# Kernel optimization log

Measured on AMD Instinct MI355X. Metric: run time of the kernel, lower is better.

Reference implementation:

```python
import jax, jax.numpy as jnp
import numpy as np

HIDDEN = 1024
H2 = HIDDEN // 2
LAYERS = 2
NUM_CONDS = 4


def _lstm_dir(x, Wih, Whh, b, reverse):
    # x: (B, T, I); Wih: (4*H2, I); Whh: (4*H2, H2); b: (4*H2,)
    B = x.shape[0]
    h2 = Whh.shape[1]
    pre = jnp.einsum('bti,gi->btg', x, Wih) + b  # precompute input contribution
    pre = jnp.swapaxes(pre, 0, 1)  # (T, B, 4*H2)
    if reverse:
        pre = pre[::-1]

    def step(carry, g_in):
        h, c = carry
        g = g_in + h @ Whh.T
        i, f, gg, o = jnp.split(g, 4, axis=-1)
        c = jax.nn.sigmoid(f) * c + jax.nn.sigmoid(i) * jnp.tanh(gg)
        h = jax.nn.sigmoid(o) * jnp.tanh(c)
        return (h, c), h

    init = (jnp.zeros((B, h2), x.dtype), jnp.zeros((B, h2), x.dtype))
    _, hs = jax.lax.scan(step, init, pre)
    if reverse:
        hs = hs[::-1]
    return jnp.swapaxes(hs, 0, 1)  # (B, T, H2)


def _bilstm(x, Wih, Whh, b):
    # Wih: (L, 2, 4*H2, I) — all layers share input width since embed_dim == hidden_dim
    out = x
    for l in range(Wih.shape[0]):
        fwd = _lstm_dir(out, Wih[l, 0], Whh[l, 0], b[l, 0], False)
        bwd = _lstm_dir(out, Wih[l, 1], Whh[l, 1], b[l, 1], True)
        out = jnp.concatenate([fwd, bwd], axis=-1)
    return out


def setup_inputs() -> dict:
    key = jax.random.key(0)
    ks = jax.random.split(key, 24)
    s = 0.02
    G = 4 * H2
    inp = {
        'question_embedding': jax.random.normal(ks[0], (32, 128, 1024), jnp.float32),
        'packed_column_embedding': jax.random.normal(ks[1], (640, 8, 1024), jnp.float32),
        'gold_num': jax.random.randint(ks[2], (32,), 0, 5),
        'gold_cols': jax.random.randint(ks[3], (32, 4), 0, 20),
        'gold_ops': jax.random.randint(ks[4], (32, 4), 0, 4),
        'num_columns': 20,
        'q_Wih': jax.random.normal(ks[5], (LAYERS, 2, G, 1024), jnp.float32) * s,
        'q_Whh': jax.random.normal(ks[6], (LAYERS, 2, G, H2), jnp.float32) * s,
        'q_b': jax.random.normal(ks[7], (LAYERS, 2, G), jnp.float32) * s,
        'c_Wih': jax.random.normal(ks[8], (LAYERS, 2, G, 1024), jnp.float32) * s,
        'c_Whh': jax.random.normal(ks[9], (LAYERS, 2, G, H2), jnp.float32) * s,
        'c_b': jax.random.normal(ks[10], (LAYERS, 2, G), jnp.float32) * s,
        'col_attn_w': jax.random.normal(ks[11], (1, HIDDEN), jnp.float32) * s,
        'col_attn_b': jnp.zeros((1,), jnp.float32),
        'ob_attn_W': jax.random.normal(ks[12], (HIDDEN, HIDDEN), jnp.float32) * s,
        'ob_attn_b': jnp.zeros((HIDDEN,), jnp.float32),
        'ob_col_W': jax.random.normal(ks[13], (HIDDEN, HIDDEN), jnp.float32) * s,
        'ob_col_b': jnp.zeros((HIDDEN,), jnp.float32),
        'q_proj_W': jax.random.normal(ks[14], (HIDDEN, HIDDEN), jnp.float32) * s,
        'q_proj_b': jnp.zeros((HIDDEN,), jnp.float32),
        'out1_W': jax.random.normal(ks[15], (HIDDEN, 3 * HIDDEN), jnp.float32) * s,
        'out1_b': jnp.zeros((HIDDEN,), jnp.float32),
        'out2_W': jax.random.normal(ks[16], (2, HIDDEN), jnp.float32) * s,
        'out2_b': jnp.zeros((2,), jnp.float32),
    }
    return inp


def _forward(question_embedding, packed_column_embedding, gold_num, gold_cols,
             num_columns, q_Wih, q_Whh, q_b, c_Wih, c_Whh, c_b,
             col_attn_w, col_attn_b, ob_attn_W, ob_attn_b, ob_col_W, ob_col_b,
             q_proj_W, q_proj_b, out1_W, out1_b, out2_W, out2_b):
    dt = question_embedding.dtype
    bs, Tq, _ = question_embedding.shape
    # compute_mask: nonzero token positions
    q_mask = (jnp.abs(question_embedding).sum(-1) != 0).astype(dt)  # (B, Tq)
    c_mask = (jnp.abs(packed_column_embedding).sum(-1) != 0).astype(dt)  # (P, Tc)

    q_enc = _bilstm(question_embedding, q_Wih, q_Whh, q_b)  # (B, Tq, H)
    c_enc = _bilstm(packed_column_embedding, c_Wih, c_Whh, c_b)  # (P, Tc, H)

    # attention-pool each column name: make_weight = masked softmax over tokens
    logits = jnp.einsum('pth,oh->pt', c_enc, col_attn_w) + col_attn_b[0]
    logits = jnp.where(c_mask > 0, logits, -jnp.inf)
    w = jax.nn.softmax(logits, axis=-1)
    col_pooled = jnp.einsum('pt,pth->ph', w, c_enc)  # (P, H)
    column_hidden = col_pooled.reshape(bs, num_columns, HIDDEN)  # (B, NC, H)

    # get_observed_column_hidden (torch.no_grad): gather gold columns, zero-pad
    K = gold_cols.shape[1]
    gn = jnp.minimum(gold_num, K)
    cond_mask = (jnp.arange(K)[None, :] < gn[:, None]).astype(dt)  # (B, K)
    observed = jnp.take_along_axis(column_hidden, gold_cols[:, :, None], axis=1)  # (B, K, H)
    observed = observed * cond_mask[..., None]
    observed = jax.lax.stop_gradient(observed)
    cond_mask = jax.lax.stop_gradient(cond_mask)

    # mm_attention over question tokens
    att_key = observed @ ob_attn_W.T + ob_attn_b  # (B, K, H)
    scores = jnp.einsum('bkh,bqh->bkq', att_key, q_enc)
    scores = jnp.where(q_mask[:, None, :] > 0, scores, -jnp.inf)
    attn = jax.nn.softmax(scores, axis=-1)
    q_hidden = jnp.einsum('bkq,bqh->bkh', attn, q_enc)  # (B, K, H)

    vec = jnp.concatenate([observed @ ob_col_W.T + ob_col_b,
                           q_hidden @ q_proj_W.T + q_proj_b], axis=-1)  # (B, K, 2H)
    # broadcast concat: (B, K, Tq, 3H)
    x = jnp.concatenate([
        jnp.broadcast_to(q_enc[:, None], (bs, K, Tq, HIDDEN)),
        jnp.broadcast_to(vec[:, :, None], (bs, K, Tq, 2 * HIDDEN)),
    ], axis=-1)
    h1 = jnp.tanh(x @ out1_W.T + out1_b)
    pos = h1 @ out2_W.T + out2_b  # (B, K, Tq, 2)

    full_mask = cond_mask[:, :, None] * q_mask[:, None, :]  # (B, K, Tq)
    pos = jnp.where(full_mask[..., None] > 0, pos, -jnp.inf)
    return pos[..., 0], pos[..., 1]


def reference(question_embedding, packed_column_embedding, gold_num, gold_cols,
              gold_ops, num_columns, q_Wih, q_Whh, q_b, c_Wih, c_Whh, c_b,
              col_attn_w, col_attn_b, ob_attn_W, ob_attn_b, ob_col_W, ob_col_b,
              q_proj_W, q_proj_b, out1_W, out1_b, out2_W, out2_b):
    # gold_ops is accepted but unused by the original forward
    return _forward(question_embedding, packed_column_embedding, gold_num, gold_cols,
                    num_columns, q_Wih, q_Whh, q_b, c_Wih, c_Whh, c_b,
                    col_attn_w, col_attn_b, ob_attn_W, ob_attn_b, ob_col_W, ob_col_b,
                    q_proj_W, q_proj_b, out1_W, out1_b, out2_W, out2_b)
```

## Files before the change

### kernel.cpp

```cpp
#include <hip/hip_runtime.h>
#include <math.h>


using f32x4 = __attribute__((ext_vector_type(4))) float;
using s16x8 = __attribute__((ext_vector_type(8))) short;
typedef unsigned long long ulong_t;

#define ASYNC_COPY16(gsrc, ldst)                                               \
  __builtin_amdgcn_global_load_lds(                                            \
      (const __attribute__((address_space(1))) void*)(gsrc),                   \
      (__attribute__((address_space(3))) void*)(ldst), 16, 0, 0)

static __device__ __forceinline__ float sigm(float x) {
  return 1.0f / (1.0f + expf(-x));
}

static __device__ __forceinline__ unsigned short f2b_one(float x) {
  unsigned int u = __float_as_uint(x);
  u = (u + 0x7FFFu + ((u >> 16) & 1u)) >> 16;
  return (unsigned short)u;
}

static __device__ __forceinline__ bool haszero16(ulong_t x) {
  return ((x - 0x0001000100010001ull) & ~x & 0x8000800080008000ull) != 0ull;
}

#define SENT64 0x7FC07FC07FC07FC0ull

__global__ __launch_bounds__(256) void f2b_kernel(
    const float* __restrict__ in, unsigned short* __restrict__ out, int n4)
{
  const int i = blockIdx.x * 256 + threadIdx.x;
  if (i >= n4) return;
  const float4 v = ((const float4*)in)[i];
  ushort4 r;
  r.x = f2b_one(v.x); r.y = f2b_one(v.y);
  r.z = f2b_one(v.z); r.w = f2b_one(v.w);
  ((ushort4*)out)[i] = r;
}

__global__ __launch_bounds__(256) void mask_kernel(
    const float* __restrict__ qe, const float* __restrict__ pce,
    float* __restrict__ qmask, float* __restrict__ cmask)
{
  const int w = threadIdx.x >> 6;
  const int lane = threadIdx.x & 63;
  const int row = blockIdx.x * 4 + w;
  const float* src = (row < 4096) ? (qe + (size_t)row * 1024)
                                  : (pce + (size_t)(row - 4096) * 1024);
  float s = 0.f;
#pragma unroll
  for (int j = 0; j < 16; ++j) s += fabsf(src[lane + j * 64]);
#pragma unroll
  for (int off = 32; off > 0; off >>= 1) s += __shfl_down(s, off, 64);
  if (lane == 0) {
    const float m = (s != 0.f) ? 1.f : 0.f;
    if (row < 4096) qmask[row] = m;
    else cmask[row - 4096] = m;
  }
}

__global__ __launch_bounds__(256) void mfma_gemm_kernel(
    const unsigned short* __restrict__ X, const unsigned short* __restrict__ W,
    const float* __restrict__ bias, float* __restrict__ C,
    int K, int ldx, int ldw, int k0w, int ldc, int c0)
{
  __shared__ unsigned short As[128 * 32];
  __shared__ unsigned short Bs[128 * 32];
  const int tid = threadIdx.x;
  const int w = tid >> 6;
  const int l = tid & 63;
  const int m0 = blockIdx.y * 128;
  const int n0 = blockIdx.x * 128;
  const int wm = (w >> 1) * 64;
  const int wn = (w & 1) * 64;

  const unsigned short* xg =
      X + (size_t)(m0 + w * 32 + (l >> 2)) * ldx + (l & 3) * 8;
  const unsigned short* wgp =
      W + (size_t)(n0 + w * 32 + (l >> 2)) * ldw + k0w + (l & 3) * 8;
  unsigned short* asb = As + w * 1024;
  unsigned short* bsb = Bs + w * 1024;

  const int fr = l & 15;
  const int fq = l >> 4;
  const unsigned short* aRd = As + (wm + fr) * 32 + fq * 8;
  const unsigned short* bRd = Bs + (wn + fr) * 32 + fq * 8;

  f32x4 acc[4][4];
#pragma unroll
  for (int i = 0; i < 4; ++i)
#pragma unroll
    for (int j = 0; j < 4; ++j) acc[i][j] = (f32x4){0.f, 0.f, 0.f, 0.f};

  for (int k0 = 0; k0 < K; k0 += 32) {
    ASYNC_COPY16(xg + k0, asb);
    ASYNC_COPY16(xg + (size_t)16 * ldx + k0, asb + 512);
    ASYNC_COPY16(wgp + k0, bsb);
    ASYNC_COPY16(wgp + (size_t)16 * ldw + k0, bsb + 512);
    __syncthreads();
    s16x8 a[4], b[4];
#pragma unroll
    for (int i = 0; i < 4; ++i) a[i] = *(const s16x8*)(aRd + i * 512);
#pragma unroll
    for (int j = 0; j < 4; ++j) b[j] = *(const s16x8*)(bRd + j * 512);
#pragma unroll
    for (int i = 0; i < 4; ++i)
#pragma unroll
      for (int j = 0; j < 4; ++j)
        acc[i][j] = __builtin_amdgcn_mfma_f32_16x16x32_bf16(
            a[i], b[j], acc[i][j], 0, 0, 0);
    __syncthreads();
  }

#pragma unroll
  for (int j = 0; j < 4; ++j) {
    const int col = n0 + wn + j * 16 + fr;
    const float bj = bias ? bias[col] : 0.f;
#pragma unroll
    for (int i = 0; i < 4; ++i) {
      const int row = m0 + wm + i * 16 + fq * 4;
#pragma unroll
      for (int r = 0; r < 4; ++r)
        C[(size_t)(row + r) * ldc + c0 + col] = acc[i][j][r] + bj;
    }
  }
}

__global__ __launch_bounds__(256) void gemm_kernel(
    const float* __restrict__ X, const float* __restrict__ W,
    const float* __restrict__ bias, float* __restrict__ C,
    int M, int N, int K, int ldx, int ldw, int k0w, int ldc, int c0)
{
  __shared__ float Xs[16][68];
  __shared__ float Ws[16][68];
  const int tid = threadIdx.x;
  const int m0 = blockIdx.y * 64;
  const int n0 = blockIdx.x * 64;
  const int lrow = tid >> 2;
  const int lkk = (tid & 3) << 2;
  const float* Xp = X + (size_t)(m0 + lrow) * ldx + lkk;
  const float* Wp = W + (size_t)(n0 + lrow) * ldw + k0w + lkk;
  const int tm = (tid >> 4) << 2;
  const int tn = (tid & 15) << 2;
  float acc[4][4];
#pragma unroll
  for (int i = 0; i < 4; ++i)
#pragma unroll
    for (int j = 0; j < 4; ++j) acc[i][j] = 0.f;

  for (int k0 = 0; k0 < K; k0 += 16) {
    const float4 xv = *(const float4*)(Xp + k0);
    const float4 wv = *(const float4*)(Wp + k0);
    Xs[lkk + 0][lrow] = xv.x; Xs[lkk + 1][lrow] = xv.y;
    Xs[lkk + 2][lrow] = xv.z; Xs[lkk + 3][lrow] = xv.w;
    Ws[lkk + 0][lrow] = wv.x; Ws[lkk + 1][lrow] = wv.y;
    Ws[lkk + 2][lrow] = wv.z; Ws[lkk + 3][lrow] = wv.w;
    __syncthreads();
#pragma unroll
    for (int kk = 0; kk < 16; ++kk) {
      const float4 a4 = *(const float4*)&Xs[kk][tm];
      const float4 b4 = *(const float4*)&Ws[kk][tn];
      const float av[4] = {a4.x, a4.y, a4.z, a4.w};
      const float bv[4] = {b4.x, b4.y, b4.z, b4.w};
#pragma unroll
      for (int i = 0; i < 4; ++i)
#pragma unroll
        for (int j = 0; j < 4; ++j) acc[i][j] += av[i] * bv[j];
    }
    __syncthreads();
  }
  float bvv[4] = {0.f, 0.f, 0.f, 0.f};
  if (bias) {
#pragma unroll
    for (int j = 0; j < 4; ++j) bvv[j] = bias[n0 + tn + j];
  }
#pragma unroll
  for (int i = 0; i < 4; ++i)
#pragma unroll
    for (int j = 0; j < 4; ++j)
      C[(size_t)(m0 + tm + i) * ldc + c0 + n0 + tn + j] = acc[i][j] + bvv[j];
}

template <int NT>
__global__ __launch_bounds__(512, 2) void lstm_seq_kernel(
    const float* __restrict__ pre,
    const unsigned short* __restrict__ whh,
    unsigned short* __restrict__ hbuf,
    float* __restrict__ out,
    int T, unsigned* __restrict__ bar, unsigned base)
{
  __shared__ float preS[NT][4][16][34];
  __shared__ float Tr[8][4][4][16];
  __shared__ unsigned short hS[NT * 16][36];
  __shared__ unsigned short hR[NT * 16][520];
  const int tid = threadIdx.x;
  const int v = tid >> 6;
  const int l = tid & 63;
  const int d = blockIdx.x >> 4;
  const int w = blockIdx.x & 15;
  const int bg = blockIdx.y;
  const int fr = l & 15;
  const int fq = l >> 4;
  const int ubase = w * 32;
  const int unit = ubase + v * 4 + fq;
  const int nbase = bg * (NT * 16);
  const size_t SLOT = (size_t)640 * 512;
  unsigned* ctr = bar + (d * 8 + bg) * 16;
  unsigned short* sl = hbuf + (size_t)d * 4 * SLOT;

  s16x8 afr[16];
  {
    const unsigned short* arow = whh + (size_t)d * 2048 * 512 +
        ((size_t)(fr >> 2) * 512 + ubase + v * 4 + (fr & 3)) * 512 + fq * 8;
#pragma unroll
    for (int kk = 0; kk < 16; ++kk)
      afr[kk] = *(const s16x8*)(arow + kk * 32);
  }

  float creg[NT];
#pragma unroll
  for (int i = 0; i < NT; ++i) creg[i] = 0.f;

  const int sc = tid & 7;
  const int sn = (tid >> 3) & 15;
  const int sg = tid >> 7;

  for (int s = 0; s < 4; ++s) {
    ulong_t* cb = (ulong_t*)(sl + (size_t)s * SLOT + (size_t)nbase * 512 + ubase);
    for (int i = tid; i < NT * 16 * 8; i += 512)
      __hip_atomic_store(cb + (size_t)(i >> 3) * 128 + (i & 7), SENT64,
                         __ATOMIC_RELAXED, __HIP_MEMORY_SCOPE_AGENT);
  }
  {
    const int tt0 = d ? (T - 1) : 0;
#pragma unroll
    for (int nt = 0; nt < NT; ++nt) {
      const int n = nbase + nt * 16 + sn;
      const float4 pv = *(const float4*)(
          pre + ((size_t)n * T + tt0) * 4096 + d * 2048 + sg * 512 + ubase +
          sc * 4);
      *(float4*)&preS[nt][sg][sn][sc * 4] = pv;
    }
  }
  __syncthreads();
  if (tid == 0) {
    __hip_atomic_fetch_add(ctr, 1u, __ATOMIC_RELAXED,
                           __HIP_MEMORY_SCOPE_AGENT);
    const unsigned target = base + 16u;
    long spins = 0;
    while (__hip_atomic_load(ctr, __ATOMIC_RELAXED,
                             __HIP_MEMORY_SCOPE_AGENT) < target) {
      __builtin_amdgcn_s_sleep(1);
      if (++spins > 2000000L) break;
    }
  }
  __syncthreads();

  float hnreg[NT];
  for (int t = 0; t < T; ++t) {
    const int tt = d ? (T - 1 - t) : t;
    const unsigned short* rd = sl + (size_t)((t + 3) & 3) * SLOT;
    unsigned short* wr = sl + (size_t)(t & 3) * SLOT;

    ulong_t u[4 * NT];
    if (t > 0) {
      const ulong_t* hq = (const ulong_t*)rd + (size_t)nbase * 128;
      bool ok = false;
      int it = 0;
      while (!ok && it < 1000000) {
#pragma unroll
        for (int i = 0; i < 2 * NT; ++i) {
          const int cid = i * 512 + tid;
          const ulong_t* p = hq + (size_t)(cid >> 6) * 128 + (cid & 63) * 2;
          u[2 * i] = __hip_atomic_load(p, __ATOMIC_RELAXED,
                                       __HIP_MEMORY_SCOPE_AGENT);
          u[2 * i + 1] = __hip_atomic_load(p + 1, __ATOMIC_RELAXED,
                                           __HIP_MEMORY_SCOPE_AGENT);
        }
        bool bad = false;
#pragma unroll
        for (int i = 0; i < 4 * NT; ++i)
          if (haszero16(u[i] ^ SENT64)) bad = true;
        ok = !bad;
        ++it;
        if (!ok && it > 8) __builtin_amdgcn_s_sleep(1);
      }
#pragma unroll
      for (int i = 0; i < 2 * NT; ++i) {
        const int cid = i * 512 + tid;
        ulong_t* dst = (ulong_t*)&hR[cid >> 6][(cid & 63) * 8];
        dst[0] = u[2 * i];
        dst[1] = u[2 * i + 1];
      }
    }
    asm volatile("" ::: "memory");
    {
      ulong_t* cb = (ulong_t*)(sl + (size_t)((t + 1) & 3) * SLOT +
                               (size_t)nbase * 512 + ubase);
      for (int i = tid; i < NT * 16 * 8; i += 512)
        __hip_atomic_store(cb + (size_t)(i >> 3) * 128 + (i & 7), SENT64,
                           __ATOMIC_RELAXED, __HIP_MEMORY_SCOPE_AGENT);
    }
    float4 pv[NT];
    if (t + 1 < T) {
      const int ttn = d ? (T - 2 - t) : (t + 1);
#pragma unroll
      for (int nt = 0; nt < NT; ++nt) {
        const int n = nbase + nt * 16 + sn;
        pv[nt] = *(const float4*)(
            pre + ((size_t)n * T + ttn) * 4096 + d * 2048 + sg * 512 + ubase +
            sc * 4);
      }
    }
    asm volatile("s_waitcnt lgkmcnt(0)" ::: "memory");
    __builtin_amdgcn_s_barrier();
    __builtin_amdgcn_sched_barrier(0);

#pragma unroll
    for (int nt = 0; nt < NT; ++nt) {
      f32x4 acc = (f32x4){0.f, 0.f, 0.f, 0.f};
      if (t > 0) {
        const unsigned short* bRd = &hR[nt * 16 + fr][fq * 8];
#pragma unroll
        for (int kk = 0; kk < 16; ++kk) {
          const s16x8 bv = *(const s16x8*)(bRd + kk * 32);
          acc = __builtin_amdgcn_mfma_f32_16x16x32_bf16(afr[kk], bv, acc,
                                                        0, 0, 0);
        }
      }
#pragma unroll
      for (int r = 0; r < 4; ++r) Tr[v][fq][r][fr] = acc[r];
      const int uu = v * 4 + fq;
      const float gi = Tr[v][0][fq][fr] + preS[nt][0][fr][uu];
      const float gf = Tr[v][1][fq][fr] + preS[nt][1][fr][uu];
      const float gg = Tr[v][2][fq][fr] + preS[nt][2][fr][uu];
      const float go = Tr[v][3][fq][fr] + preS[nt][3][fr][uu];
      const float cn = sigm(gf) * creg[nt] + sigm(gi) * tanhf(gg);
      const float hn = sigm(go) * tanhf(cn);
      creg[nt] = cn;
      hnreg[nt] = hn;
      hS[nt * 16 + fr][uu] = f2b_one(hn);
    }
    asm volatile("s_waitcnt lgkmcnt(0)" ::: "memory");
    __builtin_amdgcn_s_barrier();
    __builtin_amdgcn_sched_barrier(0);

    if (t + 1 < T) {
#pragma unroll
      for (int nt = 0; nt < NT; ++nt)
        *(float4*)&preS[nt][sg][sn][sc * 4] = pv[nt];
    }
    asm volatile("s_waitcnt vmcnt(0)" ::: "memory");
    {
      const int un = tid & 7;
      const int nl = tid >> 3;
      for (int p = nl; p < NT * 16; p += 64) {
        const ulong_t val = *(const ulong_t*)&hS[p][un * 4];
        __hip_atomic_store(
            (ulong_t*)(wr + (size_t)(nbase + p) * 512 + ubase) + un, val,
            __ATOMIC_RELAXED, __HIP_MEMORY_SCOPE_AGENT);
      }
    }
#pragma unroll
    for (int nt = 0; nt < NT; ++nt) {
      const int n = nbase + nt * 16 + fr;
      out[((size_t)n * T + tt) * 1024 + d * 512 + unit] = hnreg[nt];
    }
  }
}

__global__ __launch_bounds__(256) void colpool_kernel(
    const float* __restrict__ cenc, const float* __restrict__ caw,
    const float* __restrict__ cab, const float* __restrict__ cmask,
    float* __restrict__ colh)
{
  __shared__ float part[8][33];
  __shared__ float wbuf[8];
  const int p = blockIdx.x;
  const int t = threadIdx.x >> 5;
  const int ln = threadIdx.x & 31;
  const float* row = cenc + ((size_t)p * 8 + t) * 1024;
  float s = 0.f;
  for (int j = ln; j < 1024; j += 32) s += row[j] * caw[j];
  part[t][ln] = s;
  __syncthreads();
  if (threadIdx.x < 8) {
    float lg = 0.f;
    for (int i = 0; i < 32; ++i) lg += part[threadIdx.x][i];
    lg += cab[0];
    wbuf[threadIdx.x] = (cmask[p * 8 + threadIdx.x] > 0.f) ? lg : -INFINITY;
  }
  __syncthreads();
  if (threadIdx.x == 0) {
    float mx = -INFINITY;
    for (int i = 0; i < 8; ++i) mx = fmaxf(mx, wbuf[i]);
    float e[8];
    float sum = 0.f;
    for (int i = 0; i < 8; ++i) { e[i] = expf(wbuf[i] - mx); sum += e[i]; }
    for (int i = 0; i < 8; ++i) wbuf[i] = e[i] / sum;
  }
  __syncthreads();
  for (int h = threadIdx.x; h < 1024; h += 256) {
    float a = 0.f;
#pragma unroll
    for (int i = 0; i < 8; ++i) a += wbuf[i] * cenc[((size_t)p * 8 + i) * 1024 + h];
    colh[(size_t)p * 1024 + h] = a;
  }
}

__global__ __launch_bounds__(256) void gather_kernel(
    const float* __restrict__ colh, const int* __restrict__ gold_num,
    const int* __restrict__ gold_cols, const int* __restrict__ ncol,
    float* __restrict__ obs)
{
  const int idx = blockIdx.x * 256 + threadIdx.x;
  const int h = idx & 1023;
  const int k = (idx >> 10) & 3;
  const int b = idx >> 12;
  int gn = gold_num[b];
  if (gn > 4) gn = 4;
  const float m = (k < gn) ? 1.f : 0.f;
  const int col = gold_cols[b * 4 + k];
  const int NC = ncol[0];
  obs[idx] = m * colh[(size_t)(b * NC + col) * 1024 + h];
}

__global__ __launch_bounds__(128) void attn_kernel(
    const float* __restrict__ akey, const float* __restrict__ qenc,
    const float* __restrict__ qmask, float* __restrict__ qhid)
{
  __shared__ float ak[1024];
  __shared__ float red[128];
  __shared__ float at[128];
  const int bk = blockIdx.x;
  const int b = bk >> 2;
  const int tid = threadIdx.x;
  for (int i = tid; i < 1024; i += 128) ak[i] = akey[(size_t)bk * 1024 + i];
  __syncthreads();
  const float* qrow = qenc + ((size_t)b * 128 + tid) * 1024;
  float s = 0.f;
  for (int hh = 0; hh < 1024; hh += 4) {
    const float4 qv = *(const float4*)(qrow + hh);
    s += ak[hh] * qv.x + ak[hh + 1] * qv.y + ak[hh + 2] * qv.z + ak[hh + 3] * qv.w;
  }
  s = (qmask[b * 128 + tid] > 0.f) ? s : -INFINITY;
  at[tid] = s;
  red[tid] = s;
  __syncthreads();
  for (int off = 64; off > 0; off >>= 1) {
    if (tid < off) red[tid] = fmaxf(red[tid], red[tid + off]);
    __syncthreads();
  }
  const float mx = red[0];
  __syncthreads();
  const float e = expf(at[tid] - mx);
  red[tid] = e;
  __syncthreads();
  for (int off = 64; off > 0; off >>= 1) {
    if (tid < off) red[tid] += red[tid + off];
    __syncthreads();
  }
  const float inv = 1.f / red[0];
  __syncthreads();
  at[tid] = e * inv;
  __syncthreads();
  for (int h = tid; h < 1024; h += 128) {
    float a = 0.f;
    for (int q = 0; q < 128; ++q)
      a += at[q] * qenc[((size_t)b * 128 + q) * 1024 + h];
    qhid[(size_t)bk * 1024 + h] = a;
  }
}

__global__ __launch_bounds__(64) void final_kernel(
    const float* __restrict__ A, const float* __restrict__ Bm,
    const float* __restrict__ w2, const float* __restrict__ b2,
    const int* __restrict__ gold_num, const float* __restrict__ qmask,
    float* __restrict__ out)
{
  const int bkq = blockIdx.x;
  const int q = bkq & 127;
  const int k = (bkq >> 7) & 3;
  const int b = bkq >> 9;
  int gn = gold_num[b];
  if (gn > 4) gn = 4;
  const bool act = (k < gn) && (qmask[b * 128 + q] > 0.f);
  const int lane = threadIdx.x;
  const int obase = (b * 4 + k) * 128 + q;
  if (!act) {
    if (lane == 0) {
      out[obase] = -1e30f;
      out[16384 + obase] = -1e30f;
    }
    return;
  }
  const float* Ar = A + ((size_t)b * 128 + q) * 1024;
  const float* Br = Bm + (size_t)(b * 4 + k) * 1024;
  float s0 = 0.f, s1 = 0.f;
  for (int o = lane; o < 1024; o += 64) {
    const float v = tanhf(Ar[o] + Br[o]);
    s0 += v * w2[o];
    s1 += v * w2[1024 + o];
  }
#pragma unroll
  for (int off = 32; off > 0; off >>= 1) {
    s0 += __shfl_down(s0, off, 64);
    s1 += __shfl_down(s1, off, 64);
  }
  if (lane == 0) {
    out[obase] = s0 + b2[0];
    out[16384 + obase] = s1 + b2[1];
  }
}

extern "C" void kernel_launch(void* const* d_in, const int* in_sizes, int n_in,
                              void* d_out, int out_size, void* d_ws, size_t ws_size,
                              hipStream_t stream)
{
  const float* qe      = (const float*)d_in[0];
  const float* pce     = (const float*)d_in[1];
  const int* gold_num  = (const int*)d_in[2];
  const int* gold_cols = (const int*)d_in[3];
  const int* ncol      = (const int*)d_in[5];
  const float* q_Wih   = (const float*)d_in[6];
  const float* q_Whh   = (const float*)d_in[7];
  const float* q_b     = (const float*)d_in[8];
  const float* c_Wih   = (const float*)d_in[9];
  const float* c_Whh   = (const float*)d_in[10];
  const float* c_b     = (const float*)d_in[11];
  const float* caw     = (const float*)d_in[12];
  const float* cab     = (const float*)d_in[13];
  const float* obaW    = (const float*)d_in[14];
  const float* obab    = (const float*)d_in[15];
  const float* obcW    = (const float*)d_in[16];
  const float* obcb    = (const float*)d_in[17];
  const float* qpW     = (const float*)d_in[18];
  const float* qpb     = (const float*)d_in[19];
  const float* o1W     = (const float*)d_in[20];
  const float* o1b     = (const float*)d_in[21];
  const float* o2W     = (const float*)d_in[22];
  const float* o2b     = (const float*)d_in[23];
  float* outp = (float*)d_out;

  float* ws = (float*)d_ws;
  size_t off = 0;
  float* pre  = ws + off; off += 640UL * 8 * 4096;
  float* bufA = ws + off; off += 640UL * 8 * 1024;
  float* bufB = ws + off; off += 640UL * 8 * 1024;
  float* colh = ws + off; off += 640UL * 1024;
  float* qmask = ws + off; off += 4096;
  float* cmask = ws + off; off += 5120;
  float* obs  = ws + off; off += 131072;
  float* akey = ws + off; off += 131072;
  float* qhid = ws + off; off += 131072;
  float* vec  = ws + off; off += 262144;
  float* Bm   = ws + off; off += 131072;
  unsigned short* xb = (unsigned short*)(ws + off); off += 2621440;
  unsigned short* wb = (unsigned short*)(ws + off); off += 2097152;
  unsigned short* whhq = (unsigned short*)(ws + off); off += 2097152;
  unsigned short* whhc = (unsigned short*)(ws + off); off += 2097152;
  unsigned short* hbuf = (unsigned short*)(ws + off); off += 1310720;
  unsigned* bar = (unsigned*)(ws + off); off += 256;
  float* Amat = pre;

  const dim3 blk(256);
  auto cvt = [&](const float* src, unsigned short* dst, int n) {
    hipLaunchKernelGGL(f2b_kernel, dim3((n / 4 + 255) / 256), blk, 0, stream,
                       src, dst, n / 4);
  };

  hipMemsetAsync(bar, 0, 1024, stream);

  hipLaunchKernelGGL(mask_kernel, dim3(2304), blk, 0, stream, qe, pce, qmask, cmask);

  cvt(q_Whh, whhq, 4194304);
  cvt(c_Whh, whhc, 4194304);

  for (int l = 0; l < 2; ++l) {
    const float* xin = (l == 0) ? pce : bufA;
    float* enc = (l == 0) ? bufA : bufB;
    cvt(xin, xb, 5242880);
    cvt(c_Wih + (size_t)l * 4194304, wb, 4194304);
    hipLaunchKernelGGL(mfma_gemm_kernel, dim3(4096 / 128, 5120 / 128), blk, 0,
                       stream, xb, wb, c_b + l * 4096, pre,
                       1024, 1024, 1024, 0, 4096, 0);
    hipLaunchKernelGGL((lstm_seq_kernel<5>), dim3(32, 8), dim3(512), 0, stream,
                       pre, whhc + (size_t)l * 2 * 2048 * 512, hbuf, enc,
                       8, bar, (unsigned)(l * 16));
  }
  hipLaunchKernelGGL(colpool_kernel, dim3(640), blk, 0, stream,
                     bufB, caw, cab, cmask, colh);
  hipLaunchKernelGGL(gather_kernel, dim3(512), blk, 0, stream,
                     colh, gold_num, gold_cols, ncol, obs);

  for (int l = 0; l < 2; ++l) {
    const float* xin = (l == 0) ? qe : bufA;
    float* enc = (l == 0) ? bufA : bufB;
    cvt(xin, xb, 4194304);
    cvt(q_Wih + (size_t)l * 4194304, wb, 4194304);
    hipLaunchKernelGGL(mfma_gemm_kernel, dim3(4096 / 128, 4096 / 128), blk, 0,
                       stream, xb, wb, q_b + l * 4096, pre,
                       1024, 1024, 1024, 0, 4096, 0);
    hipLaunchKernelGGL((lstm_seq_kernel<2>), dim3(32, 1), dim3(512), 0, stream,
                       pre, whhq + (size_t)l * 2 * 2048 * 512, hbuf, enc,
                       128, bar, (unsigned)(32 + l * 16));
  }
  const float* qenc = bufB;

  hipLaunchKernelGGL(gemm_kernel, dim3(16, 2), blk, 0, stream,
                     obs, obaW, obab, akey, 128, 1024, 1024, 1024, 1024, 0, 1024, 0);
  hipLaunchKernelGGL(attn_kernel, dim3(128), dim3(128), 0, stream,
                     akey, qenc, qmask, qhid);
  hipLaunchKernelGGL(gemm_kernel, dim3(16, 2), blk, 0, stream,
                     obs, obcW, obcb, vec, 128, 1024, 1024, 1024, 1024, 0, 2048, 0);
  hipLaunchKernelGGL(gemm_kernel, dim3(16, 2), blk, 0, stream,
                     qhid, qpW, qpb, vec, 128, 1024, 1024, 1024, 1024, 0, 2048, 1024);
  cvt(qenc, xb, 4194304);
  cvt(o1W, wb, 3145728);
  hipLaunchKernelGGL(mfma_gemm_kernel, dim3(1024 / 128, 4096 / 128), blk, 0,
                     stream, xb, wb, o1b, Amat, 1024, 1024, 3072, 0, 1024, 0);
  hipLaunchKernelGGL(gemm_kernel, dim3(16, 2), blk, 0, stream,
                     vec, o1W, nullptr, Bm, 128, 1024, 2048, 2048, 3072, 1024, 1024, 0);
  hipLaunchKernelGGL(final_kernel, dim3(16384), dim3(64), 0, stream,
                     Amat, Bm, o2W, o2b, gold_num, qmask, outp);
}
```

Before: 2.162 ms.

## Replace sentinel-reset handshake with LSB parity tags and fast transcendental math

The recurrent LSTM kernel no longer rewrites sentinel NaN values into the next hidden-state slot on every step. Each bf16 hidden value now carries a parity tag in its least significant bit, which flips every three steps across a triple-buffered ring, and readers poll until every element shows the expected tag. This removes the per-step sentinel stores and one vmcnt wait. The gate nonlinearities also switch to __expf plus hardware reciprocal, and LDS rows are padded differently. The cost is one bit of bf16 mantissa in h and slightly less accurate sigmoid/tanh, and the ordering across the three-slot ring is subtle to get right.

```diff
diff --git a/kernel.cpp b/kernel.cpp
--- a/kernel.cpp
+++ b/kernel.cpp
@@ -11,8 +11,13 @@
       (const __attribute__((address_space(1))) void*)(gsrc),                   \
       (__attribute__((address_space(3))) void*)(ldst), 16, 0, 0)
 
+#define LSBM 0x0001000100010001ull
+
 static __device__ __forceinline__ float sigm(float x) {
-  return 1.0f / (1.0f + expf(-x));
+  return __builtin_amdgcn_rcpf(1.0f + __expf(-x));
+}
+static __device__ __forceinline__ float tanh_f(float x) {
+  return 1.0f - 2.0f * __builtin_amdgcn_rcpf(__expf(2.0f * x) + 1.0f);
 }
 
 static __device__ __forceinline__ unsigned short f2b_one(float x) {
@@ -20,12 +25,6 @@
   u = (u + 0x7FFFu + ((u >> 16) & 1u)) >> 16;
   return (unsigned short)u;
 }
-
-static __device__ __forceinline__ bool haszero16(ulong_t x) {
-  return ((x - 0x0001000100010001ull) & ~x & 0x8000800080008000ull) != 0ull;
-}
-
-#define SENT64 0x7FC07FC07FC07FC0ull
 
 __global__ __launch_bounds__(256) void f2b_kernel(
     const float* __restrict__ in, unsigned short* __restrict__ out, int n4)
@@ -191,9 +190,9 @@
     int T, unsigned* __restrict__ bar, unsigned base)
 {
   __shared__ float preS[NT][4][16][34];
-  __shared__ float Tr[8][4][4][16];
+  __shared__ float Tr[8][4][4][20];
   __shared__ unsigned short hS[NT * 16][36];
-  __shared__ unsigned short hR[NT * 16][520];
+  __shared__ unsigned short hR[NT * 16][528];
   const int tid = threadIdx.x;
   const int v = tid >> 6;
   const int l = tid & 63;
@@ -207,7 +206,7 @@
   const int nbase = bg * (NT * 16);
   const size_t SLOT = (size_t)640 * 512;
   unsigned* ctr = bar + (d * 8 + bg) * 16;
-  unsigned short* sl = hbuf + (size_t)d * 4 * SLOT;
+  unsigned short* sl = hbuf + (size_t)d * 3 * SLOT;
 
   s16x8 afr[16];
   {
@@ -226,10 +225,10 @@
   const int sn = (tid >> 3) & 15;
   const int sg = tid >> 7;
 
-  for (int s = 0; s < 4; ++s) {
+  for (int s = 0; s < 3; ++s) {
     ulong_t* cb = (ulong_t*)(sl + (size_t)s * SLOT + (size_t)nbase * 512 + ubase);
     for (int i = tid; i < NT * 16 * 8; i += 512)
-      __hip_atomic_store(cb + (size_t)(i >> 3) * 128 + (i & 7), SENT64,
+      __hip_atomic_store(cb + (size_t)(i >> 3) * 128 + (i & 7), LSBM,
                          __ATOMIC_RELAXED, __HIP_MEMORY_SCOPE_AGENT);
   }
   {
@@ -260,15 +259,19 @@
   float hnreg[NT];
   for (int t = 0; t < T; ++t) {
     const int tt = d ? (T - 1 - t) : t;
-    const unsigned short* rd = sl + (size_t)((t + 3) & 3) * SLOT;
-    unsigned short* wr = sl + (size_t)(t & 3) * SLOT;
-
-    ulong_t u[4 * NT];
+    const unsigned wtag = (unsigned)((t / 3) & 1);
+    unsigned short* wr = sl + (size_t)(t % 3) * SLOT;
+
     if (t > 0) {
-      const ulong_t* hq = (const ulong_t*)rd + (size_t)nbase * 128;
+      const unsigned rtag = (unsigned)(((t - 1) / 3) & 1);
+      const ulong_t want = rtag ? LSBM : 0ull;
+      const ulong_t* hq =
+          (const ulong_t*)(sl + (size_t)((t + 2) % 3) * SLOT) +
+          (size_t)nbase * 128;
+      ulong_t u[4 * NT];
       bool ok = false;
       int it = 0;
-      while (!ok && it < 1000000) {
+      while (!ok && it < 200000) {
 #pragma unroll
         for (int i = 0; i < 2 * NT; ++i) {
           const int cid = i * 512 + tid;
@@ -280,11 +283,10 @@
         }
         bool bad = false;
 #pragma unroll
-        for (int i = 0; i < 4 * NT; ++i)
-          if (haszero16(u[i] ^ SENT64)) bad = true;
+        for (int i = 0; i < 4 * NT; ++i) bad |= ((u[i] & LSBM) != want);
         ok = !bad;
         ++it;
-        if (!ok && it > 8) __builtin_amdgcn_s_sleep(1);
+        if (!ok && it > 12) __builtin_amdgcn_s_sleep(1);
       }
 #pragma unroll
       for (int i = 0; i < 2 * NT; ++i) {
@@ -294,14 +296,6 @@
         dst[1] = u[2 * i + 1];
       }
     }
-    asm volatile("" ::: "memory");
-    {
-      ulong_t* cb = (ulong_t*)(sl + (size_t)((t + 1) & 3) * SLOT +
-                               (size_t)nbase * 512 + ubase);
-      for (int i = tid; i < NT * 16 * 8; i += 512)
-        __hip_atomic_store(cb + (size_t)(i >> 3) * 128 + (i & 7), SENT64,
-                           __ATOMIC_RELAXED, __HIP_MEMORY_SCOPE_AGENT);
-    }
     float4 pv[NT];
     if (t + 1 < T) {
       const int ttn = d ? (T - 2 - t) : (t + 1);
@@ -336,11 +330,14 @@
       const float gf = Tr[v][1][fq][fr] + preS[nt][1][fr][uu];
       const float gg = Tr[v][2][fq][fr] + preS[nt][2][fr][uu];
       const float go = Tr[v][3][fq][fr] + preS[nt][3][fr][uu];
-      const float cn = sigm(gf) * creg[nt] + sigm(gi) * tanhf(gg);
-      const float hn = sigm(go) * tanhf(cn);
+      const float cn = sigm(gf) * creg[nt] + sigm(gi) * tanh_f(gg);
+      const float hn = sigm(go) * tanh_f(cn);
       creg[nt] = cn;
       hnreg[nt] = hn;
-      hS[nt * 16 + fr][uu] = f2b_one(hn);
+      hS[nt * 16 + fr][uu] =
+          (unsigned short)((f2b_one(hn) & 0xFFFEu) | wtag);
+      const int n0i = nbase + nt * 16 + fr;
+      (void)n0i;
     }
     asm volatile("s_waitcnt lgkmcnt(0)" ::: "memory");
     __builtin_amdgcn_s_barrier();
@@ -351,7 +348,6 @@
       for (int nt = 0; nt < NT; ++nt)
         *(float4*)&preS[nt][sg][sn][sc * 4] = pv[nt];
     }
-    asm volatile("s_waitcnt vmcnt(0)" ::: "memory");
     {
       const int un = tid & 7;
       const int nl = tid >> 3;
@@ -560,7 +556,7 @@
   unsigned short* wb = (unsigned short*)(ws + off); off += 2097152;
   unsigned short* whhq = (unsigned short*)(ws + off); off += 2097152;
   unsigned short* whhc = (unsigned short*)(ws + off); off += 2097152;
-  unsigned short* hbuf = (unsigned short*)(ws + off); off += 1310720;
+  unsigned short* hbuf = (unsigned short*)(ws + off); off += 983040;
   unsigned* bar = (unsigned*)(ws + off); off += 256;
   float* Amat = pre;
 
```

Measured after the change: 1.976 ms. 8.6% less time.
